# Optimization experiments

Hardware: AMD Instinct MI355X
Metric: run time of the kernel (lower is better)

Reference implementation:

```python
import jax, jax.numpy as jnp
import numpy as np
from jax.scipy.special import logsumexp

GRID_N = 512
N_ITERS = 5


def _build_grid(n):
    nH = n * (n - 1)
    E = 2 * n * (n - 1)
    P = (n - 1) * (n - 1)
    N = n * n
    pi, pj = np.meshgrid(np.arange(n - 1), np.arange(n - 1), indexing='ij')
    pi, pj = pi.ravel(), pj.ravel()
    # child edges of plaquette (i,j): top/bottom horizontal, left/right vertical
    pce = np.stack([pi * (n - 1) + pj,
                    (pi + 1) * (n - 1) + pj,
                    nH + pi * n + pj,
                    nH + pi * n + pj + 1], 1).astype(np.int32)
    epp = np.zeros((E, 2), np.int32)
    eps = np.zeros((E, 2), np.int32)
    epm = np.zeros((E, 2), np.float32)
    ev = np.zeros((E, 2), np.int32)
    hi, hj = np.meshgrid(np.arange(n), np.arange(n - 1), indexing='ij')
    hi, hj = hi.ravel(), hj.ravel()
    he = hi * (n - 1) + hj
    m = hi < n - 1
    epp[he[m], 0] = hi[m] * (n - 1) + hj[m]; epm[he[m], 0] = 1; eps[he, 0] = 0
    m = hi > 0
    epp[he[m], 1] = (hi[m] - 1) * (n - 1) + hj[m]; epm[he[m], 1] = 1; eps[he, 1] = 1
    ev[he, 0] = hi * n + hj; ev[he, 1] = hi * n + hj + 1
    vi, vj = np.meshgrid(np.arange(n - 1), np.arange(n), indexing='ij')
    vi, vj = vi.ravel(), vj.ravel()
    ve = nH + vi * n + vj
    m = vj < n - 1
    epp[ve[m], 0] = vi[m] * (n - 1) + vj[m]; epm[ve[m], 0] = 1; eps[ve, 0] = 2
    m = vj > 0
    epp[ve[m], 1] = vi[m] * (n - 1) + vj[m] - 1; epm[ve[m], 1] = 1; eps[ve, 1] = 3
    ev[ve, 0] = vi * n + vj; ev[ve, 1] = (vi + 1) * n + vj
    return epp, eps, epm, pce, ev, E, P, N


def setup_inputs() -> dict:
    n = GRID_N
    epp, eps, epm, pce, ev, E, P, N = _build_grid(n)
    key = jax.random.key(0)
    k1, k2 = jax.random.split(key)
    return {
        'log_phi_plaq': 0.5 * jax.random.normal(k1, (P, 2, 2, 2, 2), jnp.float32),
        'log_phi_edge': 0.5 * jax.random.normal(k2, (E, 2, 2), jnp.float32),
        'edge_parent_plaq': jnp.asarray(epp),
        'edge_parent_slot': jnp.asarray(eps),
        'edge_parent_mask': jnp.asarray(epm),
        'plaq_child_edge': jnp.asarray(pce),
        'edge_vars': jnp.asarray(ev),
        'n_iters': N_ITERS,
        'n_vars': N,
    }


def _forward(log_phi_plaq, log_phi_edge, epp, eps, epm, pce, ev, n_iters, n_vars):
    P = log_phi_plaq.shape[0]
    maskNN = epm[:, :, None, None]

    def edge_totals(logM):
        # sum of log-messages from (<=2) parents into each edge, plus edge factor
        g = logM[epp, eps]                      # [E,2,2,2]
        return log_phi_edge + jnp.sum(g * maskNN, axis=1)  # [E,2,2]

    def plaq_terms(logM, tot):
        n_all = tot[pce] - logM                 # [P,4,2,2]: child msg excluding this parent
        b0 = n_all[:, 0, :, :, None, None]      # top edge -> vars (a,b)
        b1 = n_all[:, 1, None, None, :, :]      # bottom  -> vars (c,d)
        b2 = n_all[:, 2, :, None, :, None]      # left    -> vars (a,c)
        b3 = n_all[:, 3, None, :, None, :]      # right   -> vars (b,d)
        S = log_phi_plaq + b0 + b1 + b2 + b3    # [P,2,2,2,2] plaquette log-belief (unnorm)
        return S, (b0, b1, b2, b3)

    def step(logM, _):
        tot = edge_totals(logM)
        S, (b0, b1, b2, b3) = plaq_terms(logM, tot)
        m0 = logsumexp(S - b0, axis=(3, 4))
        m1 = logsumexp(S - b1, axis=(1, 2))
        m2 = logsumexp(S - b2, axis=(2, 4))
        m3 = logsumexp(S - b3, axis=(1, 3))
        new = jnp.stack([m0, m1, m2, m3], axis=1)
        new = new - logsumexp(new, axis=(2, 3), keepdims=True)  # normalize messages
        return new, None

    logM0 = jnp.full((P, 4, 2, 2), -jnp.log(4.0), log_phi_plaq.dtype)
    logM, _ = jax.lax.scan(step, logM0, None, length=n_iters)

    tot = edge_totals(logM)
    log_b_e = tot - logsumexp(tot, axis=(1, 2), keepdims=True)
    S, _ = plaq_terms(logM, tot)
    log_b_p = S - logsumexp(S, axis=(1, 2, 3, 4), keepdims=True)
    b_e = jnp.exp(log_b_e)
    b_p = jnp.exp(log_b_p)

    # Kikuchi free energy: c_plaq = 1, c_edge = 1 - #parents
    c_e = 1.0 - jnp.sum(epm, axis=1)
    F = (jnp.sum(b_p * (log_b_p - log_phi_plaq))
         + jnp.sum(c_e * jnp.sum(b_e * (log_b_e - log_phi_edge), axis=(1, 2))))

    binary_marginals = b_e                      # every pair is an R1 region
    pa = b_e.sum(axis=2)                        # [E,2] marginal of first var
    pb = b_e.sum(axis=1)                        # [E,2] marginal of second var
    ones = jnp.ones((ev.shape[0],), b_e.dtype)
    node_sum = (jax.ops.segment_sum(pa, ev[:, 0], num_segments=n_vars)
                + jax.ops.segment_sum(pb, ev[:, 1], num_segments=n_vars))
    deg = (jax.ops.segment_sum(ones, ev[:, 0], num_segments=n_vars)
           + jax.ops.segment_sum(ones, ev[:, 1], num_segments=n_vars))
    unary_marginals = node_sum / deg[:, None]   # [N,2]
    return -F, unary_marginals, binary_marginals


def reference(log_phi_plaq, log_phi_edge, edge_parent_plaq, edge_parent_slot,
              edge_parent_mask, plaq_child_edge, edge_vars, n_iters, n_vars):
    return _forward(log_phi_plaq, log_phi_edge, edge_parent_plaq, edge_parent_slot,
                    edge_parent_mask, plaq_child_edge, edge_vars, n_iters, n_vars)
```

## Files before the change

kernel.cpp:

```cpp
#include <hip/hip_runtime.h>
#include <hip/hip_fp16.h>
#include <math.h>


#define CORE 22
#define REG  32
#define NTHR 1024

static __device__ __forceinline__ float4 ld4(const float* p){ return *(const float4*)p; }

static __device__ __forceinline__
float edge_store(float t0, float t1, float t2, float t3,
                 const float* peq, float* ob, bool twopar)
{
  float r = fmaxf(fmaxf(t0,t1), fmaxf(t2,t3));
  float e0=__expf(t0-r), e1=__expf(t1-r), e2=__expf(t2-r), e3=__expf(t3-r);
  float Z = e0+e1+e2+e3;
  float lse = r + __logf(Z);
  float invZ = 1.f/Z;
  float b0=e0*invZ, b1=e1*invZ, b2=e2*invZ, b3=e3*invZ;
  ob[0]=b0; ob[1]=b1; ob[2]=b2; ob[3]=b3;
  if (twopar)
    return -( b0*(t0-lse-peq[0]) + b1*(t1-lse-peq[1])
            + b2*(t2-lse-peq[2]) + b3*(t3-lse-peq[3]) );
  return 0.f;
}

__global__ __launch_bounds__(NTHR)
void fused_kernel(const float* __restrict__ phiP, const float* __restrict__ phiE,
                  float* __restrict__ outBin, float* __restrict__ Pblk,
                  int m, int n)
{
  __shared__ __half2 pln[2][8][REG*REG];
  const int r = threadIdx.x;
  const int base_i = (int)blockIdx.y*CORE - 5;
  const int base_j = (int)blockIdx.x*CORE - 5;
  const int nH = n*m;

  const int ry = r >> 5, rx = r & 31;
  const int gi = base_i + ry, gj = base_j + rx;
  const int ci = min(max(gi,0), m-1), cj = min(max(gj,0), m-1);
  const bool m0 = gi > 0, m1 = gi < m-1, m2 = gj > 0, m3 = gj < m-1;
  const int r0 = max(ry-1,0)*REG + rx;
  const int r1 = min(ry+1,REG-1)*REG + rx;
  const int r2 = ry*REG + max(rx-1,0);
  const int r3 = ry*REG + min(rx+1,REG-1);
  const bool core = (ry >= 5) && (ry < 5+CORE) && (gi < m) &&
                    (rx >= 5) && (rx < 5+CORE) && (gj < m);

  float pe[16], ph[16];
  ((float4*)pe)[0] = ld4(phiE + 4*(size_t)(ci*m+cj));
  ((float4*)pe)[1] = ld4(phiE + 4*(size_t)((ci+1)*m+cj));
  ((float4*)pe)[2] = ld4(phiE + 4*(size_t)(nH+ci*n+cj));
  ((float4*)pe)[3] = ld4(phiE + 4*(size_t)(nH+ci*n+cj+1));
  {
    const float* pp = phiP + 16*(size_t)(ci*m+cj);
    ((float4*)ph)[0]=ld4(pp);   ((float4*)ph)[1]=ld4(pp+4);
    ((float4*)ph)[2]=ld4(pp+8); ((float4*)ph)[3]=ld4(pp+12);
  }

  float outf[16];
  for (int it=0; it<5; ++it){
    const int cb = it & 1, nb = cb ^ 1;

    float na[4][4];
    if (it == 0){
      #pragma unroll
      for (int k=0;k<16;k++) na[k>>2][k&3] = pe[k];
    } else {
      __half2 a, b; float4 o;
      a = pln[cb][2][r0]; b = pln[cb][3][r0];
      o = m0 ? make_float4(__low2float(a),__high2float(a),__low2float(b),__high2float(b))
             : make_float4(0.f,0.f,0.f,0.f);
      na[0][0]=pe[0]+o.x; na[0][1]=pe[1]+o.y; na[0][2]=pe[2]+o.z; na[0][3]=pe[3]+o.w;
      a = pln[cb][0][r1]; b = pln[cb][1][r1];
      o = m1 ? make_float4(__low2float(a),__high2float(a),__low2float(b),__high2float(b))
             : make_float4(0.f,0.f,0.f,0.f);
      na[1][0]=pe[4]+o.x; na[1][1]=pe[5]+o.y; na[1][2]=pe[6]+o.z; na[1][3]=pe[7]+o.w;
      a = pln[cb][6][r2]; b = pln[cb][7][r2];
      o = m2 ? make_float4(__low2float(a),__high2float(a),__low2float(b),__high2float(b))
             : make_float4(0.f,0.f,0.f,0.f);
      na[2][0]=pe[8]+o.x; na[2][1]=pe[9]+o.y; na[2][2]=pe[10]+o.z; na[2][3]=pe[11]+o.w;
      a = pln[cb][4][r3]; b = pln[cb][5][r3];
      o = m3 ? make_float4(__low2float(a),__high2float(a),__low2float(b),__high2float(b))
             : make_float4(0.f,0.f,0.f,0.f);
      na[3][0]=pe[12]+o.x; na[3][1]=pe[13]+o.y; na[3][2]=pe[14]+o.z; na[3][3]=pe[15]+o.w;
    }

    float g[4][4];
    #pragma unroll
    for (int s=0;s<4;s++){ g[s][0]=0.f; g[s][1]=0.f; g[s][2]=0.f; g[s][3]=0.f; }
    #pragma unroll
    for (int idx=0; idx<16; ++idx){
      const int a=(idx>>3)&1, b=(idx>>2)&1, c=(idx>>1)&1, d=idx&1;
      float e = __expf(ph[idx] + na[0][(a<<1)|b] + na[1][(c<<1)|d]
                               + na[2][(a<<1)|c] + na[3][(b<<1)|d]);
      g[0][(a<<1)|b]+=e; g[1][(c<<1)|d]+=e; g[2][(a<<1)|c]+=e; g[3][(b<<1)|d]+=e;
    }
    #pragma unroll
    for (int s=0;s<4;s++){
      float c0 = __logf(g[s][0]) - na[s][0];
      outf[(s<<2)|0] = 0.f;
      #pragma unroll
      for (int k=1;k<4;k++)
        outf[(s<<2)|k] = __logf(g[s][k]) - na[s][k] - c0;
    }

    #pragma unroll
    for (int h=0; h<8; ++h)
      pln[nb][h][r] = __floats2half2_rn(outf[2*h], outf[2*h+1]);
    __syncthreads();
  }

  float contrib = 0.f;
  if (core){
    float na5[4][4];
    {
      __half2 a, b; float4 o;
      a = pln[1][2][r0]; b = pln[1][3][r0];
      o = m0 ? make_float4(__low2float(a),__high2float(a),__low2float(b),__high2float(b))
             : make_float4(0.f,0.f,0.f,0.f);
      na5[0][0]=pe[0]+o.x; na5[0][1]=pe[1]+o.y; na5[0][2]=pe[2]+o.z; na5[0][3]=pe[3]+o.w;
      a = pln[1][0][r1]; b = pln[1][1][r1];
      o = m1 ? make_float4(__low2float(a),__high2float(a),__low2float(b),__high2float(b))
             : make_float4(0.f,0.f,0.f,0.f);
      na5[1][0]=pe[4]+o.x; na5[1][1]=pe[5]+o.y; na5[1][2]=pe[6]+o.z; na5[1][3]=pe[7]+o.w;
      a = pln[1][6][r2]; b = pln[1][7][r2];
      o = m2 ? make_float4(__low2float(a),__high2float(a),__low2float(b),__high2float(b))
             : make_float4(0.f,0.f,0.f,0.f);
      na5[2][0]=pe[8]+o.x; na5[2][1]=pe[9]+o.y; na5[2][2]=pe[10]+o.z; na5[2][3]=pe[11]+o.w;
      a = pln[1][4][r3]; b = pln[1][5][r3];
      o = m3 ? make_float4(__low2float(a),__high2float(a),__low2float(b),__high2float(b))
             : make_float4(0.f,0.f,0.f,0.f);
      na5[3][0]=pe[12]+o.x; na5[3][1]=pe[13]+o.y; na5[3][2]=pe[14]+o.z; na5[3][3]=pe[15]+o.w;
    }
    {
      float S[16]; float Z=0.f;
      #pragma unroll
      for (int idx=0; idx<16; ++idx){
        const int a=(idx>>3)&1, b=(idx>>2)&1, c=(idx>>1)&1, d=idx&1;
        S[idx] = ph[idx] + na5[0][(a<<1)|b] + na5[1][(c<<1)|d]
                         + na5[2][(a<<1)|c] + na5[3][(b<<1)|d];
      }
      float Es[16];
      #pragma unroll
      for (int idx=0; idx<16; ++idx){ Es[idx]=__expf(S[idx]); Z+=Es[idx]; }
      float lse  = __logf(Z);
      float invZ = 1.f/Z;
      #pragma unroll
      for (int idx=0; idx<16; ++idx)
        contrib += (Es[idx]*invZ) * (S[idx]-lse-ph[idx]);
    }
    contrib += edge_store(na5[0][0]+outf[0], na5[0][1]+outf[1],
                          na5[0][2]+outf[2], na5[0][3]+outf[3],
                          pe+0, outBin + 4*(size_t)(gi*m+gj), gi>0);
    contrib += edge_store(na5[2][0]+outf[8],  na5[2][1]+outf[9],
                          na5[2][2]+outf[10], na5[2][3]+outf[11],
                          pe+8, outBin + 4*(size_t)(nH+gi*n+gj), gj>0);
    if (gi == m-1)
      edge_store(pe[4]+outf[4], pe[5]+outf[5], pe[6]+outf[6], pe[7]+outf[7],
                 pe+4, outBin + 4*(size_t)((gi+1)*m+gj), false);
    if (gj == m-1)
      edge_store(pe[12]+outf[12], pe[13]+outf[13], pe[14]+outf[14], pe[15]+outf[15],
                 pe+12, outBin + 4*(size_t)(nH+gi*n+gj+1), false);
  }

  __syncthreads();
  float* red = (float*)&pln[0][0][0];
  #pragma unroll
  for (int off=32; off>0; off>>=1) contrib += __shfl_down(contrib, off, 64);
  if ((r & 63) == 0) red[r >> 6] = contrib;
  __syncthreads();
  if (r < 16){
    float v = red[r];
    #pragma unroll
    for (int off=8; off>0; off>>=1) v += __shfl_down(v, off, 16);
    if (r == 0) Pblk[blockIdx.y*gridDim.x + blockIdx.x] = v;
  }
}

__global__ __launch_bounds__(256)
void unary_kernel(const float* __restrict__ bin, float* __restrict__ out,
                  const float* __restrict__ Pblk, int m, int n, int nblk)
{
  if (blockIdx.x == 0 && blockIdx.y == 0){
    __shared__ float red[256];
    int tid = threadIdx.y*64 + threadIdx.x;
    float s = 0.f;
    for (int idx = tid; idx < nblk; idx += 256) s += Pblk[idx];
    red[tid] = s; __syncthreads();
    #pragma unroll
    for (int st=128; st>0; st>>=1){
      if (tid < st) red[tid] += red[tid+st];
      __syncthreads();
    }
    if (tid == 0) out[0] = -red[0];
  }
  int j = blockIdx.x*64 + threadIdx.x;
  int i = blockIdx.y*4  + threadIdx.y;
  if (i >= n || j >= n) return;
  const int nH = n*m;
  float s0=0.f, s1=0.f, deg=0.f;
  if (j < m){ const float* b = bin + 4*(size_t)(i*m+j);        s0 += b[0]+b[1]; s1 += b[2]+b[3]; deg+=1.f; }
  if (j > 0){ const float* b = bin + 4*(size_t)(i*m+j-1);      s0 += b[0]+b[2]; s1 += b[1]+b[3]; deg+=1.f; }
  if (i < m){ const float* b = bin + 4*(size_t)(nH+i*n+j);     s0 += b[0]+b[1]; s1 += b[2]+b[3]; deg+=1.f; }
  if (i > 0){ const float* b = bin + 4*(size_t)(nH+(i-1)*n+j); s0 += b[0]+b[2]; s1 += b[1]+b[3]; deg+=1.f; }
  float inv = 1.f/deg;
  size_t v = (size_t)i*n + j;
  out[1+2*v]   = s0*inv;
  out[1+2*v+1] = s1*inv;
}

extern "C" void kernel_launch(void* const* d_in, const int* in_sizes, int n_in,
                              void* d_out, int out_size, void* d_ws, size_t ws_size,
                              hipStream_t stream)
{
  const float* phiP = (const float*)d_in[0];
  const float* phiE = (const float*)d_in[1];
  int P  = in_sizes[0] / 16;
  int m  = (int)(sqrt((double)P) + 0.5);
  int n  = m + 1;
  int N  = n * n;
  float* out  = (float*)d_out;
  float* Pblk = (float*)d_ws;

  int tiles = (m + CORE - 1) / CORE;
  float* outBin = out + 1 + 2*(size_t)N;
  fused_kernel<<<dim3(tiles, tiles), dim3(NTHR), 0, stream>>>(phiP, phiE, outBin, Pblk, m, n);
  unary_kernel<<<dim3((n+63)/64, (n+3)/4), dim3(64,4), 0, stream>>>(outBin, out, Pblk, m, n, tiles*tiles);
}
```

Baseline: 149.4 us.

## Run message passing in exponential domain to replace per-state exp/log with products

Potentials are exponentiated once at load, and the iterative loop keeps messages in linear space. Each of the 16 joint states now costs multiplies instead of an exp, and messages are max-normalized with a reciprocal instead of taking four logs. Leave-one-out products replace the log subtraction of incoming messages. The free-energy terms are rebuilt from logs of the linear quantities. This trades transcendental throughput for risk of underflow or overflow, and messages still round-trip through half precision in shared memory.

```diff
diff --git a/kernel.cpp b/kernel.cpp
--- a/kernel.cpp
+++ b/kernel.cpp
@@ -8,23 +8,7 @@
 #define NTHR 1024
 
 static __device__ __forceinline__ float4 ld4(const float* p){ return *(const float4*)p; }
-
-static __device__ __forceinline__
-float edge_store(float t0, float t1, float t2, float t3,
-                 const float* peq, float* ob, bool twopar)
-{
-  float r = fmaxf(fmaxf(t0,t1), fmaxf(t2,t3));
-  float e0=__expf(t0-r), e1=__expf(t1-r), e2=__expf(t2-r), e3=__expf(t3-r);
-  float Z = e0+e1+e2+e3;
-  float lse = r + __logf(Z);
-  float invZ = 1.f/Z;
-  float b0=e0*invZ, b1=e1*invZ, b2=e2*invZ, b3=e3*invZ;
-  ob[0]=b0; ob[1]=b1; ob[2]=b2; ob[3]=b3;
-  if (twopar)
-    return -( b0*(t0-lse-peq[0]) + b1*(t1-lse-peq[1])
-            + b2*(t2-lse-peq[2]) + b3*(t3-lse-peq[3]) );
-  return 0.f;
-}
+static __device__ __forceinline__ float rcpf(float x){ return __builtin_amdgcn_rcpf(x); }
 
 __global__ __launch_bounds__(NTHR)
 void fused_kernel(const float* __restrict__ phiP, const float* __restrict__ phiE,
@@ -48,43 +32,49 @@
   const bool core = (ry >= 5) && (ry < 5+CORE) && (gi < m) &&
                     (rx >= 5) && (rx < 5+CORE) && (gj < m);
 
-  float pe[16], ph[16];
-  ((float4*)pe)[0] = ld4(phiE + 4*(size_t)(ci*m+cj));
-  ((float4*)pe)[1] = ld4(phiE + 4*(size_t)((ci+1)*m+cj));
-  ((float4*)pe)[2] = ld4(phiE + 4*(size_t)(nH+ci*n+cj));
-  ((float4*)pe)[3] = ld4(phiE + 4*(size_t)(nH+ci*n+cj+1));
+  float peE[16], phE[16];
   {
+    float4 v;
+    v = ld4(phiE + 4*(size_t)(ci*m+cj));
+    peE[0]=__expf(v.x); peE[1]=__expf(v.y); peE[2]=__expf(v.z); peE[3]=__expf(v.w);
+    v = ld4(phiE + 4*(size_t)((ci+1)*m+cj));
+    peE[4]=__expf(v.x); peE[5]=__expf(v.y); peE[6]=__expf(v.z); peE[7]=__expf(v.w);
+    v = ld4(phiE + 4*(size_t)(nH+ci*n+cj));
+    peE[8]=__expf(v.x); peE[9]=__expf(v.y); peE[10]=__expf(v.z); peE[11]=__expf(v.w);
+    v = ld4(phiE + 4*(size_t)(nH+ci*n+cj+1));
+    peE[12]=__expf(v.x); peE[13]=__expf(v.y); peE[14]=__expf(v.z); peE[15]=__expf(v.w);
     const float* pp = phiP + 16*(size_t)(ci*m+cj);
-    ((float4*)ph)[0]=ld4(pp);   ((float4*)ph)[1]=ld4(pp+4);
-    ((float4*)ph)[2]=ld4(pp+8); ((float4*)ph)[3]=ld4(pp+12);
-  }
-
-  float outf[16];
+    #pragma unroll
+    for (int h=0; h<4; ++h){
+      v = ld4(pp + 4*h);
+      phE[4*h+0]=__expf(v.x); phE[4*h+1]=__expf(v.y);
+      phE[4*h+2]=__expf(v.z); phE[4*h+3]=__expf(v.w);
+    }
+  }
+
+  float outp[16];
   for (int it=0; it<5; ++it){
     const int cb = it & 1, nb = cb ^ 1;
 
     float na[4][4];
     if (it == 0){
       #pragma unroll
-      for (int k=0;k<16;k++) na[k>>2][k&3] = pe[k];
+      for (int k=0;k<16;k++) na[k>>2][k&3] = peE[k];
     } else {
       __half2 a, b; float4 o;
+      const float4 one = make_float4(1.f,1.f,1.f,1.f);
       a = pln[cb][2][r0]; b = pln[cb][3][r0];
-      o = m0 ? make_float4(__low2float(a),__high2float(a),__low2float(b),__high2float(b))
-             : make_float4(0.f,0.f,0.f,0.f);
-      na[0][0]=pe[0]+o.x; na[0][1]=pe[1]+o.y; na[0][2]=pe[2]+o.z; na[0][3]=pe[3]+o.w;
+      o = m0 ? make_float4(__low2float(a),__high2float(a),__low2float(b),__high2float(b)) : one;
+      na[0][0]=peE[0]*o.x; na[0][1]=peE[1]*o.y; na[0][2]=peE[2]*o.z; na[0][3]=peE[3]*o.w;
       a = pln[cb][0][r1]; b = pln[cb][1][r1];
-      o = m1 ? make_float4(__low2float(a),__high2float(a),__low2float(b),__high2float(b))
-             : make_float4(0.f,0.f,0.f,0.f);
-      na[1][0]=pe[4]+o.x; na[1][1]=pe[5]+o.y; na[1][2]=pe[6]+o.z; na[1][3]=pe[7]+o.w;
+      o = m1 ? make_float4(__low2float(a),__high2float(a),__low2float(b),__high2float(b)) : one;
+      na[1][0]=peE[4]*o.x; na[1][1]=peE[5]*o.y; na[1][2]=peE[6]*o.z; na[1][3]=peE[7]*o.w;
       a = pln[cb][6][r2]; b = pln[cb][7][r2];
-      o = m2 ? make_float4(__low2float(a),__high2float(a),__low2float(b),__high2float(b))
-             : make_float4(0.f,0.f,0.f,0.f);
-      na[2][0]=pe[8]+o.x; na[2][1]=pe[9]+o.y; na[2][2]=pe[10]+o.z; na[2][3]=pe[11]+o.w;
+      o = m2 ? make_float4(__low2float(a),__high2float(a),__low2float(b),__high2float(b)) : one;
+      na[2][0]=peE[8]*o.x; na[2][1]=peE[9]*o.y; na[2][2]=peE[10]*o.z; na[2][3]=peE[11]*o.w;
       a = pln[cb][4][r3]; b = pln[cb][5][r3];
-      o = m3 ? make_float4(__low2float(a),__high2float(a),__low2float(b),__high2float(b))
-             : make_float4(0.f,0.f,0.f,0.f);
-      na[3][0]=pe[12]+o.x; na[3][1]=pe[13]+o.y; na[3][2]=pe[14]+o.z; na[3][3]=pe[15]+o.w;
+      o = m3 ? make_float4(__low2float(a),__high2float(a),__low2float(b),__high2float(b)) : one;
+      na[3][0]=peE[12]*o.x; na[3][1]=peE[13]*o.y; na[3][2]=peE[14]*o.z; na[3][3]=peE[15]*o.w;
     }
 
     float g[4][4];
@@ -93,76 +83,107 @@
     #pragma unroll
     for (int idx=0; idx<16; ++idx){
       const int a=(idx>>3)&1, b=(idx>>2)&1, c=(idx>>1)&1, d=idx&1;
-      float e = __expf(ph[idx] + na[0][(a<<1)|b] + na[1][(c<<1)|d]
-                               + na[2][(a<<1)|c] + na[3][(b<<1)|d]);
-      g[0][(a<<1)|b]+=e; g[1][(c<<1)|d]+=e; g[2][(a<<1)|c]+=e; g[3][(b<<1)|d]+=e;
+      const int ab=(a<<1)|b, cd=(c<<1)|d, ac=(a<<1)|c, bd=(b<<1)|d;
+      float E = (na[0][ab]*na[1][cd]) * (na[2][ac]*na[3][bd]) * phE[idx];
+      g[0][ab]+=E; g[1][cd]+=E; g[2][ac]+=E; g[3][bd]+=E;
     }
     #pragma unroll
     for (int s=0;s<4;s++){
-      float c0 = __logf(g[s][0]) - na[s][0];
-      outf[(s<<2)|0] = 0.f;
-      #pragma unroll
-      for (int k=1;k<4;k++)
-        outf[(s<<2)|k] = __logf(g[s][k]) - na[s][k] - c0;
+      float l1=na[s][0], l2=l1*na[s][1], l3=l2*na[s][2];
+      float q2=na[s][3], q1=q2*na[s][2], q0=q1*na[s][1];
+      float o0=g[s][0]*q0, o1=g[s][1]*l1*q1, o2=g[s][2]*l2*q2, o3=g[s][3]*l3;
+      float inv = rcpf(fmaxf(fmaxf(o0,o1), fmaxf(o2,o3)));
+      outp[(s<<2)|0]=o0*inv; outp[(s<<2)|1]=o1*inv;
+      outp[(s<<2)|2]=o2*inv; outp[(s<<2)|3]=o3*inv;
     }
 
     #pragma unroll
     for (int h=0; h<8; ++h)
-      pln[nb][h][r] = __floats2half2_rn(outf[2*h], outf[2*h+1]);
+      pln[nb][h][r] = __floats2half2_rn(outp[2*h], outp[2*h+1]);
     __syncthreads();
   }
 
   float contrib = 0.f;
   if (core){
-    float na5[4][4];
+    float o5_0[4], o5_2[4], naE5[4][4];
     {
       __half2 a, b; float4 o;
+      const float4 one = make_float4(1.f,1.f,1.f,1.f);
       a = pln[1][2][r0]; b = pln[1][3][r0];
-      o = m0 ? make_float4(__low2float(a),__high2float(a),__low2float(b),__high2float(b))
-             : make_float4(0.f,0.f,0.f,0.f);
-      na5[0][0]=pe[0]+o.x; na5[0][1]=pe[1]+o.y; na5[0][2]=pe[2]+o.z; na5[0][3]=pe[3]+o.w;
+      o = m0 ? make_float4(__low2float(a),__high2float(a),__low2float(b),__high2float(b)) : one;
+      o5_0[0]=o.x; o5_0[1]=o.y; o5_0[2]=o.z; o5_0[3]=o.w;
+      naE5[0][0]=peE[0]*o.x; naE5[0][1]=peE[1]*o.y; naE5[0][2]=peE[2]*o.z; naE5[0][3]=peE[3]*o.w;
       a = pln[1][0][r1]; b = pln[1][1][r1];
-      o = m1 ? make_float4(__low2float(a),__high2float(a),__low2float(b),__high2float(b))
-             : make_float4(0.f,0.f,0.f,0.f);
-      na5[1][0]=pe[4]+o.x; na5[1][1]=pe[5]+o.y; na5[1][2]=pe[6]+o.z; na5[1][3]=pe[7]+o.w;
+      o = m1 ? make_float4(__low2float(a),__high2float(a),__low2float(b),__high2float(b)) : one;
+      naE5[1][0]=peE[4]*o.x; naE5[1][1]=peE[5]*o.y; naE5[1][2]=peE[6]*o.z; naE5[1][3]=peE[7]*o.w;
       a = pln[1][6][r2]; b = pln[1][7][r2];
-      o = m2 ? make_float4(__low2float(a),__high2float(a),__low2float(b),__high2float(b))
-             : make_float4(0.f,0.f,0.f,0.f);
-      na5[2][0]=pe[8]+o.x; na5[2][1]=pe[9]+o.y; na5[2][2]=pe[10]+o.z; na5[2][3]=pe[11]+o.w;
+      o = m2 ? make_float4(__low2float(a),__high2float(a),__low2float(b),__high2float(b)) : one;
+      o5_2[0]=o.x; o5_2[1]=o.y; o5_2[2]=o.z; o5_2[3]=o.w;
+      naE5[2][0]=peE[8]*o.x; naE5[2][1]=peE[9]*o.y; naE5[2][2]=peE[10]*o.z; naE5[2][3]=peE[11]*o.w;
       a = pln[1][4][r3]; b = pln[1][5][r3];
-      o = m3 ? make_float4(__low2float(a),__high2float(a),__low2float(b),__high2float(b))
-             : make_float4(0.f,0.f,0.f,0.f);
-      na5[3][0]=pe[12]+o.x; na5[3][1]=pe[13]+o.y; na5[3][2]=pe[14]+o.z; na5[3][3]=pe[15]+o.w;
-    }
-    {
-      float S[16]; float Z=0.f;
+      o = m3 ? make_float4(__low2float(a),__high2float(a),__low2float(b),__high2float(b)) : one;
+      naE5[3][0]=peE[12]*o.x; naE5[3][1]=peE[13]*o.y; naE5[3][2]=peE[14]*o.z; naE5[3][3]=peE[15]*o.w;
+    }
+    {
+      float Ln[4][4];
+      #pragma unroll
+      for (int s=0;s<4;s++)
+        #pragma unroll
+        for (int k=0;k<4;k++)
+          Ln[s][k] = __logf(fmaxf(naE5[s][k], 1e-30f));
+      float Z=0.f, accT=0.f;
       #pragma unroll
       for (int idx=0; idx<16; ++idx){
         const int a=(idx>>3)&1, b=(idx>>2)&1, c=(idx>>1)&1, d=idx&1;
-        S[idx] = ph[idx] + na5[0][(a<<1)|b] + na5[1][(c<<1)|d]
-                         + na5[2][(a<<1)|c] + na5[3][(b<<1)|d];
+        const int ab=(a<<1)|b, cd=(c<<1)|d, ac=(a<<1)|c, bd=(b<<1)|d;
+        float E = (naE5[0][ab]*naE5[1][cd]) * (naE5[2][ac]*naE5[3][bd]) * phE[idx];
+        float T = (Ln[0][ab]+Ln[1][cd]) + (Ln[2][ac]+Ln[3][bd]);
+        Z += E; accT = fmaf(E, T, accT);
       }
-      float Es[16];
-      #pragma unroll
-      for (int idx=0; idx<16; ++idx){ Es[idx]=__expf(S[idx]); Z+=Es[idx]; }
-      float lse  = __logf(Z);
-      float invZ = 1.f/Z;
-      #pragma unroll
-      for (int idx=0; idx<16; ++idx)
-        contrib += (Es[idx]*invZ) * (S[idx]-lse-ph[idx]);
-    }
-    contrib += edge_store(na5[0][0]+outf[0], na5[0][1]+outf[1],
-                          na5[0][2]+outf[2], na5[0][3]+outf[3],
-                          pe+0, outBin + 4*(size_t)(gi*m+gj), gi>0);
-    contrib += edge_store(na5[2][0]+outf[8],  na5[2][1]+outf[9],
-                          na5[2][2]+outf[10], na5[2][3]+outf[11],
-                          pe+8, outBin + 4*(size_t)(nH+gi*n+gj), gj>0);
-    if (gi == m-1)
-      edge_store(pe[4]+outf[4], pe[5]+outf[5], pe[6]+outf[6], pe[7]+outf[7],
-                 pe+4, outBin + 4*(size_t)((gi+1)*m+gj), false);
-    if (gj == m-1)
-      edge_store(pe[12]+outf[12], pe[13]+outf[13], pe[14]+outf[14], pe[15]+outf[15],
-                 pe+12, outBin + 4*(size_t)(nH+gi*n+gj+1), false);
+      contrib += accT*rcpf(Z) - __logf(Z);
+    }
+    {
+      float P0=naE5[0][0]*outp[0], P1=naE5[0][1]*outp[1],
+            P2=naE5[0][2]*outp[2], P3=naE5[0][3]*outp[3];
+      float Zt=P0+P1+P2+P3, izt=rcpf(Zt);
+      float* ob = outBin + 4*(size_t)(gi*m+gj);
+      ob[0]=P0*izt; ob[1]=P1*izt; ob[2]=P2*izt; ob[3]=P3*izt;
+      if (gi>0){
+        float q0=__logf(fmaxf(o5_0[0]*outp[0],1e-30f));
+        float q1=__logf(fmaxf(o5_0[1]*outp[1],1e-30f));
+        float q2=__logf(fmaxf(o5_0[2]*outp[2],1e-30f));
+        float q3=__logf(fmaxf(o5_0[3]*outp[3],1e-30f));
+        contrib += __logf(Zt) - (P0*q0+P1*q1+P2*q2+P3*q3)*izt;
+      }
+    }
+    {
+      float P0=naE5[2][0]*outp[8],  P1=naE5[2][1]*outp[9],
+            P2=naE5[2][2]*outp[10], P3=naE5[2][3]*outp[11];
+      float Zt=P0+P1+P2+P3, izt=rcpf(Zt);
+      float* ob = outBin + 4*(size_t)(nH+gi*n+gj);
+      ob[0]=P0*izt; ob[1]=P1*izt; ob[2]=P2*izt; ob[3]=P3*izt;
+      if (gj>0){
+        float q0=__logf(fmaxf(o5_2[0]*outp[8], 1e-30f));
+        float q1=__logf(fmaxf(o5_2[1]*outp[9], 1e-30f));
+        float q2=__logf(fmaxf(o5_2[2]*outp[10],1e-30f));
+        float q3=__logf(fmaxf(o5_2[3]*outp[11],1e-30f));
+        contrib += __logf(Zt) - (P0*q0+P1*q1+P2*q2+P3*q3)*izt;
+      }
+    }
+    if (gi == m-1){
+      float P0=naE5[1][0]*outp[4], P1=naE5[1][1]*outp[5],
+            P2=naE5[1][2]*outp[6], P3=naE5[1][3]*outp[7];
+      float izt=rcpf(P0+P1+P2+P3);
+      float* ob = outBin + 4*(size_t)((gi+1)*m+gj);
+      ob[0]=P0*izt; ob[1]=P1*izt; ob[2]=P2*izt; ob[3]=P3*izt;
+    }
+    if (gj == m-1){
+      float P0=naE5[3][0]*outp[12], P1=naE5[3][1]*outp[13],
+            P2=naE5[3][2]*outp[14], P3=naE5[3][3]*outp[15];
+      float izt=rcpf(P0+P1+P2+P3);
+      float* ob = outBin + 4*(size_t)(nH+gi*n+gj+1);
+      ob[0]=P0*izt; ob[1]=P1*izt; ob[2]=P2*izt; ob[3]=P3*izt;
+    }
   }
 
   __syncthreads();
```

After: 154.9 us. +3.7%, slower.
